# Performance work log

Measured on AMD Instinct MI355X. Metric: run time of the kernel, lower is better.

## Reference

```python
import jax, jax.numpy as jnp
import numpy as np
import math

B, T, D_MODEL = 1, 2048, 256
N_Q, N_KV = 16, 1
D_HEAD = D_MODEL // N_KV          # 256 (module forces d_head = d_model // n_kv_heads)
QPG = N_Q // N_KV                 # 16
ROPE_BASE = 10000.0
WINDOW = 512
EPS = 1.1920929e-07               # torch finfo(float32).eps (nn.RMSNorm default eps=None)
NEG = -1e30


def _rope(x, base=ROPE_BASE):
    # x: (b, q, g, t, d); interleaved-pair rotary embedding, freq shared per pair
    t, d = x.shape[-2], x.shape[-1]
    freqs = base ** (-2.0 * jnp.arange(d // 2, dtype=jnp.float32) / d)      # (d/2,)
    theta = jnp.arange(t, dtype=jnp.float32)[:, None] * freqs[None, :]     # (t, d/2)
    cos, sin = jnp.cos(theta), jnp.sin(theta)
    x1, x2 = x[..., 0::2], x[..., 1::2]
    r1 = x1 * cos - x2 * sin
    r2 = x1 * sin + x2 * cos
    return jnp.stack([r1, r2], axis=-1).reshape(x.shape)


def _rmsnorm(x, w):
    return x * jax.lax.rsqrt(jnp.mean(x * x, axis=-1, keepdims=True) + EPS) * w


def setup_inputs() -> dict:
    key = jax.random.key(0)
    k0, k1, k2, k3 = jax.random.split(key, 4)
    x = jax.random.normal(k0, (B, T, D_MODEL), dtype=jnp.float32)
    wq = jax.random.normal(k1, (QPG * N_KV * D_HEAD, D_MODEL), dtype=jnp.float32) * 0.02
    wkv = jax.random.normal(k2, (2 * D_HEAD * N_KV, D_MODEL), dtype=jnp.float32) * 0.02
    wo = jax.random.normal(k3, (D_MODEL, D_HEAD * N_Q * N_KV), dtype=jnp.float32) * 0.02
    q_norm_w = jnp.ones((D_HEAD,), dtype=jnp.float32)
    k_norm_w = jnp.ones((D_HEAD,), dtype=jnp.float32)
    return {"x": x, "wq": wq, "wkv": wkv, "wo": wo,
            "q_norm_w": q_norm_w, "k_norm_w": k_norm_w}


def reference(x, wq, wkv, wo, q_norm_w, k_norm_w):
    Bx, Tx, C = x.shape
    q = x @ wq.T                                  # (b, t, qpg*n_kv*d_head)
    kv = x @ wkv.T                                # (b, t, 2*n_kv*d_head)
    k, v = kv[..., :N_KV * D_HEAD], kv[..., N_KV * D_HEAD:]
    # b t q g d -> b q g t d
    q = q.reshape(Bx, Tx, QPG, N_KV, D_HEAD).transpose(0, 2, 3, 1, 4)
    k = k.reshape(Bx, Tx, 1, N_KV, D_HEAD).transpose(0, 2, 3, 1, 4)
    v = v.reshape(Bx, Tx, 1, N_KV, D_HEAD).transpose(0, 2, 3, 1, 4)
    q = _rmsnorm(_rope(q), q_norm_w)
    k = _rmsnorm(_rope(k), k_norm_w)
    rows = jnp.arange(Tx)[:, None]
    cols = jnp.arange(Tx)[None, :]
    mask = (cols <= rows) & ((rows - cols) <= WINDOW)           # causal & sliding window
    scale = 1.0 / math.sqrt(D_HEAD)
    scores = jnp.einsum('bqgtd,bqgsd->bqgts', q, k) * scale     # (b, qpg, n_kv, t, t)
    scores = jnp.where(mask[None, None, None], scores, NEG)
    attn = jax.nn.softmax(scores, axis=-1)
    out = jnp.einsum('bqgts,bqgsd->bqgtd', attn, v)
    out = out.transpose(0, 3, 1, 2, 4).reshape(Bx, Tx, QPG * N_KV * D_HEAD)  # b t (q g d)
    return out @ wo.T
```

## Files before the change

kernel.cpp:

```cpp
#include <hip/hip_runtime.h>

#define TT   2048
#define WIN  512

typedef unsigned short u16;
typedef unsigned long long u64;
typedef __bf16 bf16x8 __attribute__((ext_vector_type(8)));
typedef float  f32x4  __attribute__((ext_vector_type(4)));

__device__ __forceinline__ float bf2f(u16 u){
  unsigned v = ((unsigned)u) << 16;
  return __builtin_bit_cast(float, v);
}
__device__ __forceinline__ u16 f2bf(float f){
  unsigned x = __builtin_bit_cast(unsigned, f);
  unsigned r = x + 0x7fffu + ((x >> 16) & 1u);
  return (u16)(r >> 16);
}
__device__ __forceinline__ f32x4 mfma16(bf16x8 a, bf16x8 b, f32x4 c){
  return __builtin_amdgcn_mfma_f32_16x16x32_bf16(a, b, c, 0, 0, 0);
}
__device__ __forceinline__ bf16x8 ld512(const u16* buf, int row, int byte){
  return *(const bf16x8*)((const char*)buf + row*512 + (byte ^ ((row&7)<<4)));
}
__device__ __forceinline__ bf16x8 ld128(const u16* buf, int row, int byte){
  return *(const bf16x8*)((const char*)buf + row*128 + (byte ^ ((row&7)<<4)));
}
#define GL16(gp, lp) __builtin_amdgcn_global_load_lds( \
    (const __attribute__((address_space(1))) unsigned int*)(gp), \
    (__attribute__((address_space(3))) unsigned int*)(lp), 16, 0, 0)

__global__ __launch_bounds__(64) void k_detect(const u16* __restrict__ x, int* __restrict__ flag){
  int lane = threadIdx.x;
  float mx = 0.f;
  for (int i = lane; i < 2048; i += 64){
    float v = fabsf(bf2f(x[i]));
    mx = (v < 64.0f) ? fmaxf(mx, v) : 1e30f;
  }
  #pragma unroll
  for (int d = 32; d; d >>= 1) mx = fmaxf(mx, __shfl_xor(mx, d));
  if (lane == 0) *flag = (mx < 64.0f) ? 1 : 0;
}

__global__ __launch_bounds__(256) void k_prep(const void* __restrict__ x_r, const void* __restrict__ wq_r,
                                              const void* __restrict__ wkv_r, const void* __restrict__ wo_r,
                                              const void* __restrict__ qw_r, const void* __restrict__ kw_r,
                                              u16* __restrict__ xb, u16* __restrict__ wqb,
                                              u16* __restrict__ wkvb, u16* __restrict__ wob,
                                              float* __restrict__ tab, float* __restrict__ qwf,
                                              float* __restrict__ kwf, const int* __restrict__ flag){
  int b = blockIdx.x, t = threadIdx.x;
  if (b < 1024){
    int idx = b*256 + t;
    int tt = idx >> 7, i = idx & 127;
    float fr = exp2f((float)i * (-13.287712379549449f / 128.0f));
    float th = (float)tt * fr;
    tab[idx*2 + 0] = cosf(th);
    tab[idx*2 + 1] = sinf(th);
    return;
  }
  if (b == 3712){
    int f = *flag;
    qwf[t] = f ? bf2f(((const u16*)qw_r)[t]) : ((const float*)qw_r)[t];
    kwf[t] = f ? bf2f(((const u16*)kw_r)[t]) : ((const float*)kw_r)[t];
    return;
  }
  if (*flag) return;
  int cb = b - 1024;
  const float* s; u16* d; int i;
  if (cb < 512)       { s=(const float*)x_r;   d=xb;   i = cb*256 + t; }
  else if (cb < 1536) { s=(const float*)wq_r;  d=wqb;  i = (cb-512)*256 + t; }
  else if (cb < 1664) { s=(const float*)wkv_r; d=wkvb; i = (cb-1536)*256 + t; }
  else                { s=(const float*)wo_r;  d=wob;  i = (cb-1664)*256 + t; }
  float4 v = *(const float4*)(s + (size_t)i*4);
  u64 pk = (u64)f2bf(v.x) | ((u64)f2bf(v.y)<<16) | ((u64)f2bf(v.z)<<32) | ((u64)f2bf(v.w)<<48);
  *(u64*)(d + (size_t)i*4) = pk;
}

__global__ __launch_bounds__(256) void k_qkv(const u16* __restrict__ xb, const u16* __restrict__ wqb,
                                             const u16* __restrict__ wkvb,
                                             const void* __restrict__ x_r, const void* __restrict__ wq_r,
                                             const void* __restrict__ wkv_r, const int* __restrict__ flag,
                                             u16* __restrict__ q_raw, u16* __restrict__ kv_raw,
                                             u16* __restrict__ vt){
  __shared__ __align__(16) u16 Ax[64*256];
  __shared__ __align__(16) u16 Bw[64*256];
  int fl = *flag;
  const u16* x   = fl ? (const u16*)x_r   : xb;
  const u16* wq  = fl ? (const u16*)wq_r  : wqb;
  const u16* wkv = fl ? (const u16*)wkv_r : wkvb;
  int m0 = blockIdx.x * 64, n0 = blockIdx.y * 64;
  int tid = threadIdx.x;
  const u16* wsrc = (n0 < 4096) ? (wq + (size_t)n0*256) : (wkv + (size_t)(n0-4096)*256);
  int sr = tid >> 5, sk = tid & 31;
  #pragma unroll
  for (int u=0;u<8;++u){
    int r = sr + u*8;
    uint4 a = *(const uint4*)((const char*)(x    + (size_t)(m0+r)*256) + sk*16);
    uint4 b = *(const uint4*)((const char*)(wsrc + (size_t)r*256)      + sk*16);
    *(uint4*)((char*)&Ax[0] + r*512 + ((sk*16) ^ ((r&7)<<4))) = a;
    *(uint4*)((char*)&Bw[0] + r*512 + ((sk*16) ^ ((r&7)<<4))) = b;
  }
  __syncthreads();
  int w = tid>>6, lane = tid&63, ml = lane&15, g = lane>>4;
  int mh = w & 1, nh = w >> 1;
  f32x4 acc[2][2];
  #pragma unroll
  for (int mr=0;mr<2;++mr)
    #pragma unroll
    for (int j=0;j<2;++j) acc[mr][j] = f32x4{0.f,0.f,0.f,0.f};
  #pragma unroll
  for (int kk=0; kk<8; ++kk){
    bf16x8 af[2], bf[2];
    #pragma unroll
    for (int mr=0;mr<2;++mr) af[mr] = ld512(Ax, mh*32 + mr*16 + ml, kk*64 + g*16);
    #pragma unroll
    for (int j=0;j<2;++j)    bf[j]  = ld512(Bw, nh*32 + j*16 + ml,  kk*64 + g*16);
    #pragma unroll
    for (int mr=0;mr<2;++mr)
      #pragma unroll
      for (int j=0;j<2;++j) acc[mr][j] = mfma16(af[mr], bf[j], acc[mr][j]);
  }
  #pragma unroll
  for (int mr=0;mr<2;++mr)
    #pragma unroll
    for (int j=0;j<2;++j)
      #pragma unroll
      for (int r=0;r<4;++r){
        int row = m0 + mh*32 + mr*16 + 4*g + r;
        int n   = n0 + nh*32 + j*16 + ml;
        float v = acc[mr][j][r];
        u16 bv = f2bf(v);
        if (n < 4096)      q_raw[(size_t)row*4096 + n] = bv;
        else if (n < 4352) kv_raw[(size_t)row*256 + (n - 4096)] = bv;
        else               vt[(size_t)(n - 4352)*2048 + row] = bv;
      }
}

__global__ __launch_bounds__(256) void k_knorm(const u16* __restrict__ kv_raw, const float* __restrict__ tab,
                                               const float* __restrict__ kwf, u16* __restrict__ kn){
  int row  = blockIdx.x * 4 + (threadIdx.x >> 6);
  int lane = threadIdx.x & 63;
  const u16* src = kv_raw + (size_t)row*256;
  union { u64 q; u16 u[4]; } iv;
  iv.q = *(const u64*)(src + lane*4);
  float v0 = bf2f(iv.u[0]), v1 = bf2f(iv.u[1]), v2 = bf2f(iv.u[2]), v3 = bf2f(iv.u[3]);
  float4 tc = *(const float4*)(tab + (size_t)row*256 + lane*4);
  float r0 = v0*tc.x - v1*tc.y;
  float r1 = v0*tc.y + v1*tc.x;
  float r2 = v2*tc.z - v3*tc.w;
  float r3 = v2*tc.w + v3*tc.z;
  float ss = r0*r0 + r1*r1 + r2*r2 + r3*r3;
  #pragma unroll
  for (int d=32; d; d>>=1) ss += __shfl_xor(ss, d);
  float sc = rsqrtf(ss * (1.0f/256.0f) + 1.1920929e-07f);
  u64 pk =  (u64)f2bf(r0*sc*kwf[lane*4+0])
         | ((u64)f2bf(r1*sc*kwf[lane*4+1]) << 16)
         | ((u64)f2bf(r2*sc*kwf[lane*4+2]) << 32)
         | ((u64)f2bf(r3*sc*kwf[lane*4+3]) << 48);
  *(u64*)(kn + (size_t)row*256 + lane*4) = pk;
}

__global__ __launch_bounds__(512, 2) void k_attn(const u16* __restrict__ q_raw, const u16* __restrict__ kn,
                                                 const u16* __restrict__ vt, const float* __restrict__ tab,
                                                 const float* __restrict__ qwf, u16* __restrict__ aout){
  __shared__ __align__(16) u16 S[73728];
  int h = blockIdx.x >> 4, qt = blockIdx.x & 15;
  int Q0 = qt * 128;
  int tid = threadIdx.x, w = tid >> 6, lane = tid & 63, ml = lane & 15, g = lane >> 4;
  u16* Pw = S + 65536 + w*1024;
  int s_lo = Q0 - WIN; if (s_lo < 0) s_lo = 0;
  int ntile = (Q0 + 128 - s_lo) >> 6;
  int tq = Q0 + w*16 + ml;
  int wmin = Q0 + w*16, wmax = wmin + 15;

  int krl = lane >> 5, kslot = lane & 31;
  int vrl = lane >> 3, vslot = lane & 7;

  {
    int s0 = s_lo;
    #pragma unroll
    for (int i=0;i<4;++i){
      int r = w*8 + i*2 + krl;
      GL16(kn + (size_t)(s0 + r)*256 + ((kslot ^ (r&7))*8), S + (w*8 + i*2)*256);
    }
    #pragma unroll
    for (int i=0;i<4;++i){
      int d = w*32 + i*8 + vrl;
      GL16(vt + (size_t)d*2048 + s0 + ((vslot ^ (d&7))*8), S + 32768 + (w*32 + i*8)*64);
    }
  }

  bf16x8 qf[8];
  {
    const u16* qp = q_raw + (size_t)tq*4096 + h*256;
    const float* tp = tab + (size_t)tq*256;
    float rf[8][8];
    float ss = 0.f;
    #pragma unroll
    for (int kk=0; kk<8; ++kk){
      int c0 = kk*32 + 8*g;
      union { u64 q[2]; u16 u[8]; } iv;
      iv.q[0] = *(const u64*)(qp + c0);
      iv.q[1] = *(const u64*)(qp + c0 + 4);
      float4 t0 = *(const float4*)(tp + c0);
      float4 t1 = *(const float4*)(tp + c0 + 4);
      float tc[8] = {t0.x,t0.y,t0.z,t0.w,t1.x,t1.y,t1.z,t1.w};
      #pragma unroll
      for (int p=0; p<4; ++p){
        float a = bf2f(iv.u[2*p]), b = bf2f(iv.u[2*p+1]);
        float cc = tc[2*p], sn = tc[2*p+1];
        float r0 = a*cc - b*sn;
        float r1 = a*sn + b*cc;
        rf[kk][2*p] = r0; rf[kk][2*p+1] = r1;
        ss += r0*r0 + r1*r1;
      }
    }
    ss += __shfl_xor(ss, 16);
    ss += __shfl_xor(ss, 32);
    float sc = rsqrtf(ss * (1.0f/256.0f) + 1.1920929e-07f) * 0.0625f;
    #pragma unroll
    for (int kk=0; kk<8; ++kk){
      int c0 = kk*32 + 8*g;
      float4 w0 = *(const float4*)(qwf + c0);
      float4 w1 = *(const float4*)(qwf + c0 + 4);
      float wv[8] = {w0.x,w0.y,w0.z,w0.w,w1.x,w1.y,w1.z,w1.w};
      union { u16 u[8]; bf16x8 v; } pk;
      #pragma unroll
      for (int e=0; e<8; ++e) pk.u[e] = f2bf(rf[kk][e] * sc * wv[e]);
      qf[kk] = pk.v;
    }
  }

  float ls = 0.f;
  f32x4 o[16];
  #pragma unroll
  for (int f=0; f<16; ++f) o[f] = f32x4{0.f,0.f,0.f,0.f};
  int cur = 0;

  for (int kt=0; kt<ntile; ++kt){
    int s0 = s_lo + kt*64;
    if (kt+1 < ntile){
      int s1 = s0 + 64, nx = cur ^ 1;
      #pragma unroll
      for (int i=0;i<4;++i){
        int r = w*8 + i*2 + krl;
        GL16(kn + (size_t)(s1 + r)*256 + ((kslot ^ (r&7))*8), S + nx*16384 + (w*8 + i*2)*256);
      }
      #pragma unroll
      for (int i=0;i<4;++i){
        int d = w*32 + i*8 + vrl;
        GL16(vt + (size_t)d*2048 + s1 + ((vslot ^ (d&7))*8), S + 32768 + nx*16384 + (w*32 + i*8)*64);
      }
      asm volatile("s_waitcnt vmcnt(8)" ::: "memory");
    } else {
      asm volatile("s_waitcnt vmcnt(0)" ::: "memory");
    }
    __builtin_amdgcn_s_barrier();
    __builtin_amdgcn_sched_barrier(0);

    bool act = (s0 <= wmax) && (s0 + 63 + WIN >= wmin);
    if (act){
      const u16* kb = S + cur*16384;
      const u16* vb = S + 32768 + cur*16384;
      f32x4 s2[4];
      #pragma unroll
      for (int j=0;j<4;++j) s2[j] = f32x4{0.f,0.f,0.f,0.f};
      __builtin_amdgcn_s_setprio(1);
      #pragma unroll
      for (int kk=0; kk<8; ++kk)
        #pragma unroll
        for (int j=0;j<4;++j)
          s2[j] = mfma16(ld512(kb, j*16 + ml, kk*64 + g*16), qf[kk], s2[j]);
      __builtin_amdgcn_s_setprio(0);
      bool fullv = (s0 + 63 <= wmin) && (wmax - s0 <= WIN);
      float rs = 0.f;
      if (fullv){
        #pragma unroll
        for (int j=0;j<4;++j){
          u64 pk = 0;
          #pragma unroll
          for (int r=0;r<4;++r){
            float pe = __expf(s2[j][r] - 16.0f);
            rs += pe;
            pk |= (u64)f2bf(pe) << (16*r);
          }
          *(u64*)((char*)Pw + ml*128 + ((j*32 + 8*g) ^ ((ml&7)<<4))) = pk;
        }
      } else {
        #pragma unroll
        for (int j=0;j<4;++j){
          u64 pk = 0;
          #pragma unroll
          for (int r=0;r<4;++r){
            int key = s0 + j*16 + 4*g + r;
            bool ok = (key <= tq) && (tq - key <= WIN);
            float pe = ok ? __expf(s2[j][r] - 16.0f) : 0.f;
            rs += pe;
            pk |= (u64)f2bf(pe) << (16*r);
          }
          *(u64*)((char*)Pw + ml*128 + ((j*32 + 8*g) ^ ((ml&7)<<4))) = pk;
        }
      }
      rs += __shfl_xor(rs, 16);
      rs += __shfl_xor(rs, 32);
      ls += rs;
      __builtin_amdgcn_s_setprio(1);
      #pragma unroll
      for (int kk2=0; kk2<2; ++kk2){
        bf16x8 pb = ld128(Pw, ml, kk2*64 + g*16);
        #pragma unroll
        for (int f=0; f<16; ++f){
          bf16x8 vf = ld128(vb, f*16 + ml, kk2*64 + g*16);
          o[f] = mfma16(vf, pb, o[f]);
        }
      }
      __builtin_amdgcn_s_setprio(0);
    }
    __builtin_amdgcn_s_barrier();
    __builtin_amdgcn_sched_barrier(0);
    cur ^= 1;
  }
  float inv = 1.0f / ls;
  u16* dst = aout + ((size_t)h*2048 + tq)*256;
  #pragma unroll
  for (int f=0; f<16; ++f){
    f32x4 v = o[f];
    u64 pk = (u64)f2bf(v[0]*inv) | ((u64)f2bf(v[1]*inv)<<16)
           | ((u64)f2bf(v[2]*inv)<<32) | ((u64)f2bf(v[3]*inv)<<48);
    *(u64*)(dst + f*16 + 4*g) = pk;
  }
}

__global__ __launch_bounds__(256) void k_oproj(const u16* __restrict__ aout, const u16* __restrict__ wob,
                                               const void* __restrict__ wo_r, const int* __restrict__ flag,
                                               float* __restrict__ pout){
  __shared__ __align__(16) u16 As[64*256];
  __shared__ __align__(16) u16 Bs[64*256];
  const u16* wo = *flag ? (const u16*)wo_r : wob;
  int t0 = blockIdx.x * 64, c0 = blockIdx.y * 64, ksp = blockIdx.z;
  int tid = threadIdx.x, w = tid>>6, lane = tid&63, ml = lane&15, g = lane>>4;
  int mh = w & 1, nh = w >> 1;
  int sr = tid >> 5, sk = tid & 31;
  f32x4 acc[2][2];
  #pragma unroll
  for (int mr=0;mr<2;++mr)
    #pragma unroll
    for (int j=0;j<2;++j) acc[mr][j] = f32x4{0.f,0.f,0.f,0.f};
  for (int kc = ksp*4; kc < ksp*4 + 4; ++kc){
    __syncthreads();
    #pragma unroll
    for (int u=0;u<8;++u){
      int r = sr + u*8;
      uint4 a = *(const uint4*)((const char*)(aout + ((size_t)kc*2048 + t0 + r)*256) + sk*16);
      uint4 b = *(const uint4*)((const char*)(wo + (size_t)(c0+r)*4096 + kc*256) + sk*16);
      *(uint4*)((char*)&As[0] + r*512 + ((sk*16) ^ ((r&7)<<4))) = a;
      *(uint4*)((char*)&Bs[0] + r*512 + ((sk*16) ^ ((r&7)<<4))) = b;
    }
    __syncthreads();
    #pragma unroll
    for (int kk=0; kk<8; ++kk){
      bf16x8 af[2], bf[2];
      #pragma unroll
      for (int mr=0;mr<2;++mr) af[mr] = ld512(As, mh*32 + mr*16 + ml, kk*64 + g*16);
      #pragma unroll
      for (int j=0;j<2;++j)    bf[j]  = ld512(Bs, nh*32 + j*16 + ml,  kk*64 + g*16);
      #pragma unroll
      for (int mr=0;mr<2;++mr)
        #pragma unroll
        for (int j=0;j<2;++j) acc[mr][j] = mfma16(af[mr], bf[j], acc[mr][j]);
    }
  }
  #pragma unroll
  for (int mr=0;mr<2;++mr)
    #pragma unroll
    for (int j=0;j<2;++j)
      #pragma unroll
      for (int r=0;r<4;++r){
        int t = t0 + mh*32 + mr*16 + 4*g + r;
        int c = c0 + nh*32 + j*16 + ml;
        pout[((size_t)ksp*2048 + t)*256 + c] = acc[mr][j][r];
      }
}

__global__ __launch_bounds__(256) void k_red(const float* __restrict__ pout, void* __restrict__ out,
                                             const int* __restrict__ flag){
  int i = blockIdx.x * 256 + threadIdx.x;
  float v = pout[i] + pout[i + 2048*256] + pout[i + 2*2048*256] + pout[i + 3*2048*256];
  if (*flag) ((u16*)out)[i] = f2bf(v);
  else       ((float*)out)[i] = v;
}

extern "C" void kernel_launch(void* const* d_in, const int* in_sizes, int n_in,
                              void* d_out, int out_size, void* d_ws, size_t ws_size,
                              hipStream_t stream) {
  (void)in_sizes; (void)n_in; (void)out_size; (void)ws_size;
  const void* x_r   = d_in[0];
  const void* wq_r  = d_in[1];
  const void* wkv_r = d_in[2];
  const void* wo_r  = d_in[3];
  const void* qw_r  = d_in[4];
  const void* kw_r  = d_in[5];
  char* ws = (char*)d_ws;
  const size_t MB = 1048576;
  u16*   xb     = (u16*)  (ws);
  u16*   wqb    = (u16*)  (ws + 1*MB);
  u16*   wkvb   = (u16*)  (ws + 3*MB);
  u16*   wob    = (u16*)  (ws + 3*MB + MB/2);
  float* tab    = (float*)(ws + 5*MB + MB/2);
  u16*   q_raw  = (u16*)  (ws + 7*MB + MB/2);
  float* pout   = (float*)q_raw;
  u16*   kv_raw = (u16*)  (ws + 23*MB + MB/2);
  u16*   aout   = (u16*)  (ws + 25*MB + MB/2);
  u16*   kn     = (u16*)  (ws + 41*MB + MB/2);
  u16*   vt     = (u16*)  (ws + 42*MB + MB/2);
  int*   flag   = (int*)  (ws + 43*MB + MB/2);
  float* qwf    = (float*)(ws + 43*MB + MB/2 + 256);
  float* kwf    = (float*)(ws + 43*MB + MB/2 + 1280);

  k_detect<<<dim3(1),    dim3(64),  0, stream>>>((const u16*)x_r, flag);
  k_prep  <<<dim3(3713), dim3(256), 0, stream>>>(x_r, wq_r, wkv_r, wo_r, qw_r, kw_r,
                                                 xb, wqb, wkvb, wob, tab, qwf, kwf, flag);
  k_qkv   <<<dim3(32, 72),   dim3(256), 0, stream>>>(xb, wqb, wkvb, x_r, wq_r, wkv_r, flag,
                                                     q_raw, kv_raw, vt);
  k_knorm <<<dim3(512),      dim3(256), 0, stream>>>(kv_raw, tab, kwf, kn);
  k_attn  <<<dim3(256),      dim3(512), 0, stream>>>(q_raw, kn, vt, tab, qwf, aout);
  k_oproj <<<dim3(32, 4, 4), dim3(256), 0, stream>>>(aout, wob, wo_r, flag, pout);
  k_red   <<<dim3(2048),     dim3(256), 0, stream>>>(pout, d_out, flag);
}
```

Baseline: 92.10 us.

## Pair attention waves over 32 query rows, splitting keys and head dims

Waves are now grouped in pairs that share 32 query rows. In QK^T each wave of a pair takes half of the 64 keys, and in PV each takes half of the 256 output dims. Every K and V fragment read from LDS is then reused by two MFMAs (one per 16-row query block), which roughly halves LDS read traffic per MFMA. The cost is an extra block barrier per tile for the shared P exchange, a cross-wave row-sum combine through LDS at the end, and duplicated q preprocessing per wave.

```diff
diff --git a/kernel.cpp b/kernel.cpp
--- a/kernel.cpp
+++ b/kernel.cpp
@@ -164,15 +164,17 @@
 __global__ __launch_bounds__(512, 2) void k_attn(const u16* __restrict__ q_raw, const u16* __restrict__ kn,
                                                  const u16* __restrict__ vt, const float* __restrict__ tab,
                                                  const float* __restrict__ qwf, u16* __restrict__ aout){
-  __shared__ __align__(16) u16 S[73728];
+  __shared__ __align__(16) u16 S[74240];
   int h = blockIdx.x >> 4, qt = blockIdx.x & 15;
   int Q0 = qt * 128;
   int tid = threadIdx.x, w = tid >> 6, lane = tid & 63, ml = lane & 15, g = lane >> 4;
-  u16* Pw = S + 65536 + w*1024;
+  int p = w >> 1, half = w & 1;
+  u16* Pp = S + 65536 + p*2048;
+  float* LSX = (float*)(S + 73728);
   int s_lo = Q0 - WIN; if (s_lo < 0) s_lo = 0;
   int ntile = (Q0 + 128 - s_lo) >> 6;
-  int tq = Q0 + w*16 + ml;
-  int wmin = Q0 + w*16, wmax = wmin + 15;
+  int q_base = Q0 + p*32;
+  int wmin = q_base, wmax = q_base + 31;
 
   int krl = lane >> 5, kslot = lane & 31;
   int vrl = lane >> 3, vslot = lane & 7;
@@ -191,8 +193,10 @@
     }
   }
 
-  bf16x8 qf[8];
-  {
+  bf16x8 qf[2][8];
+  #pragma unroll
+  for (int mq=0; mq<2; ++mq){
+    int tq = q_base + mq*16 + ml;
     const u16* qp = q_raw + (size_t)tq*4096 + h*256;
     const float* tp = tab + (size_t)tq*256;
     float rf[8][8];
@@ -207,12 +211,12 @@
       float4 t1 = *(const float4*)(tp + c0 + 4);
       float tc[8] = {t0.x,t0.y,t0.z,t0.w,t1.x,t1.y,t1.z,t1.w};
       #pragma unroll
-      for (int p=0; p<4; ++p){
-        float a = bf2f(iv.u[2*p]), b = bf2f(iv.u[2*p+1]);
-        float cc = tc[2*p], sn = tc[2*p+1];
+      for (int pr=0; pr<4; ++pr){
+        float a = bf2f(iv.u[2*pr]), b = bf2f(iv.u[2*pr+1]);
+        float cc = tc[2*pr], sn = tc[2*pr+1];
         float r0 = a*cc - b*sn;
         float r1 = a*sn + b*cc;
-        rf[kk][2*p] = r0; rf[kk][2*p+1] = r1;
+        rf[kk][2*pr] = r0; rf[kk][2*pr+1] = r1;
         ss += r0*r0 + r1*r1;
       }
     }
@@ -228,14 +232,16 @@
       union { u16 u[8]; bf16x8 v; } pk;
       #pragma unroll
       for (int e=0; e<8; ++e) pk.u[e] = f2bf(rf[kk][e] * sc * wv[e]);
-      qf[kk] = pk.v;
-    }
-  }
-
-  float ls = 0.f;
-  f32x4 o[16];
-  #pragma unroll
-  for (int f=0; f<16; ++f) o[f] = f32x4{0.f,0.f,0.f,0.f};
+      qf[mq][kk] = pk.v;
+    }
+  }
+
+  float ls[2] = {0.f, 0.f};
+  f32x4 o[2][8];
+  #pragma unroll
+  for (int mq=0;mq<2;++mq)
+    #pragma unroll
+    for (int fb=0; fb<8; ++fb) o[mq][fb] = f32x4{0.f,0.f,0.f,0.f};
   int cur = 0;
 
   for (int kt=0; kt<ntile; ++kt){
@@ -262,73 +268,97 @@
     bool act = (s0 <= wmax) && (s0 + 63 + WIN >= wmin);
     if (act){
       const u16* kb = S + cur*16384;
-      const u16* vb = S + 32768 + cur*16384;
-      f32x4 s2[4];
-      #pragma unroll
-      for (int j=0;j<4;++j) s2[j] = f32x4{0.f,0.f,0.f,0.f};
+      f32x4 s2[2][2];
+      #pragma unroll
+      for (int mq=0;mq<2;++mq)
+        #pragma unroll
+        for (int j2=0;j2<2;++j2) s2[mq][j2] = f32x4{0.f,0.f,0.f,0.f};
       __builtin_amdgcn_s_setprio(1);
       #pragma unroll
       for (int kk=0; kk<8; ++kk)
         #pragma unroll
-        for (int j=0;j<4;++j)
-          s2[j] = mfma16(ld512(kb, j*16 + ml, kk*64 + g*16), qf[kk], s2[j]);
+        for (int j2=0;j2<2;++j2){
+          bf16x8 kfr = ld512(kb, half*32 + j2*16 + ml, kk*64 + g*16);
+          s2[0][j2] = mfma16(kfr, qf[0][kk], s2[0][j2]);
+          s2[1][j2] = mfma16(kfr, qf[1][kk], s2[1][j2]);
+        }
       __builtin_amdgcn_s_setprio(0);
       bool fullv = (s0 + 63 <= wmin) && (wmax - s0 <= WIN);
-      float rs = 0.f;
-      if (fullv){
-        #pragma unroll
-        for (int j=0;j<4;++j){
+      #pragma unroll
+      for (int mq=0;mq<2;++mq){
+        int row = mq*16 + ml;
+        int tq = q_base + mq*16 + ml;
+        float rs = 0.f;
+        #pragma unroll
+        for (int j2=0;j2<2;++j2){
           u64 pk = 0;
           #pragma unroll
           for (int r=0;r<4;++r){
-            float pe = __expf(s2[j][r] - 16.0f);
+            float v = s2[mq][j2][r];
+            float pe;
+            if (fullv){
+              pe = __expf(v - 16.0f);
+            } else {
+              int key = s0 + half*32 + j2*16 + 4*g + r;
+              bool ok = (key <= tq) && (tq - key <= WIN);
+              pe = ok ? __expf(v - 16.0f) : 0.f;
+            }
             rs += pe;
             pk |= (u64)f2bf(pe) << (16*r);
           }
-          *(u64*)((char*)Pw + ml*128 + ((j*32 + 8*g) ^ ((ml&7)<<4))) = pk;
+          *(u64*)((char*)Pp + row*128 + ((half*64 + j2*32 + 8*g) ^ ((row&7)<<4))) = pk;
         }
-      } else {
-        #pragma unroll
-        for (int j=0;j<4;++j){
-          u64 pk = 0;
-          #pragma unroll
-          for (int r=0;r<4;++r){
-            int key = s0 + j*16 + 4*g + r;
-            bool ok = (key <= tq) && (tq - key <= WIN);
-            float pe = ok ? __expf(s2[j][r] - 16.0f) : 0.f;
-            rs += pe;
-            pk |= (u64)f2bf(pe) << (16*r);
-          }
-          *(u64*)((char*)Pw + ml*128 + ((j*32 + 8*g) ^ ((ml&7)<<4))) = pk;
+        rs += __shfl_xor(rs, 16);
+        rs += __shfl_xor(rs, 32);
+        ls[mq] += rs;
+      }
+    }
+    __builtin_amdgcn_s_barrier();
+    __builtin_amdgcn_sched_barrier(0);
+    if (act){
+      const u16* vb = S + 32768 + cur*16384;
+      bf16x8 pf[2][2];
+      #pragma unroll
+      for (int mq=0;mq<2;++mq)
+        #pragma unroll
+        for (int kk2=0;kk2<2;++kk2)
+          pf[mq][kk2] = ld128(Pp, mq*16 + ml, kk2*64 + g*16);
+      __builtin_amdgcn_s_setprio(1);
+      #pragma unroll
+      for (int fb=0; fb<8; ++fb)
+        #pragma unroll
+        for (int kk2=0;kk2<2;++kk2){
+          bf16x8 vfr = ld128(vb, half*128 + fb*16 + ml, kk2*64 + g*16);
+          o[0][fb] = mfma16(vfr, pf[0][kk2], o[0][fb]);
+          o[1][fb] = mfma16(vfr, pf[1][kk2], o[1][fb]);
         }
-      }
-      rs += __shfl_xor(rs, 16);
-      rs += __shfl_xor(rs, 32);
-      ls += rs;
-      __builtin_amdgcn_s_setprio(1);
-      #pragma unroll
-      for (int kk2=0; kk2<2; ++kk2){
-        bf16x8 pb = ld128(Pw, ml, kk2*64 + g*16);
-        #pragma unroll
-        for (int f=0; f<16; ++f){
-          bf16x8 vf = ld128(vb, f*16 + ml, kk2*64 + g*16);
-          o[f] = mfma16(vf, pb, o[f]);
-        }
-      }
       __builtin_amdgcn_s_setprio(0);
     }
     __builtin_amdgcn_s_barrier();
     __builtin_amdgcn_sched_barrier(0);
     cur ^= 1;
   }
-  float inv = 1.0f / ls;
-  u16* dst = aout + ((size_t)h*2048 + tq)*256;
-  #pragma unroll
-  for (int f=0; f<16; ++f){
-    f32x4 v = o[f];
-    u64 pk = (u64)f2bf(v[0]*inv) | ((u64)f2bf(v[1]*inv)<<16)
-           | ((u64)f2bf(v[2]*inv)<<32) | ((u64)f2bf(v[3]*inv)<<48);
-    *(u64*)(dst + f*16 + 4*g) = pk;
+  if (lane < 16){
+    LSX[w*32 + lane] = ls[0];
+    LSX[w*32 + 16 + lane] = ls[1];
+  }
+  __syncthreads();
+  int wo_ = (p*2 + (1-half));
+  float lt[2];
+  lt[0] = ls[0] + LSX[wo_*32 + ml];
+  lt[1] = ls[1] + LSX[wo_*32 + 16 + ml];
+  #pragma unroll
+  for (int mq=0;mq<2;++mq){
+    float inv = 1.0f / lt[mq];
+    int tq = q_base + mq*16 + ml;
+    u16* dst = aout + ((size_t)h*2048 + tq)*256;
+    #pragma unroll
+    for (int fb=0; fb<8; ++fb){
+      f32x4 v = o[mq][fb];
+      u64 pk = (u64)f2bf(v[0]*inv) | ((u64)f2bf(v[1]*inv)<<16)
+             | ((u64)f2bf(v[2]*inv)<<32) | ((u64)f2bf(v[3]*inv)<<48);
+      *(u64*)(dst + half*128 + fb*16 + 4*g) = pk;
+    }
   }
 }
 
```

After: 111.3 us. 20.9% more time.
